# Kernel tuning notes

Hardware: AMD Instinct MI355X
Metric: run time of the kernel (lower is better)

Reference implementation:

```python
import jax, jax.numpy as jnp
import numpy as np

B, S, D = 4, 4096, 2048
K, H = 64, 32
HD = K // H  # 2
LN_EPS = 1e-5


def setup_inputs() -> dict:
    key = jax.random.key(0)
    ks = jax.random.split(key, 8)
    def xavier(k, shape):
        fan_in, fan_out = shape[1], shape[0]
        lim = float(np.sqrt(6.0 / (fan_in + fan_out)))
        return jax.random.uniform(k, shape, jnp.float32, -lim, lim)
    return {
        "x": jax.random.normal(ks[0], (B, S, D), jnp.float32),
        "norm_w": jnp.ones((D,), jnp.float32),
        "norm_b": jnp.zeros((D,), jnp.float32),
        "qkv_w": xavier(ks[1], (3 * K, D)),
        "qkv_b": jnp.zeros((3 * K,), jnp.float32),
        "fm_w": xavier(ks[2], (HD, HD)),
        "fm_b": jnp.zeros((HD,), jnp.float32),
        "out_w": xavier(ks[3], (D, K)),
        "out_b": jnp.zeros((D,), jnp.float32),
    }


def reference(x, norm_w, norm_b, qkv_w, qkv_b, fm_w, fm_b, out_w, out_b):
    # LayerNorm
    mu = jnp.mean(x, axis=-1, keepdims=True)
    var = jnp.var(x, axis=-1, keepdims=True)
    xn = (x - mu) * jax.lax.rsqrt(var + LN_EPS) * norm_w + norm_b
    # QKV projection: [B,S,3K]
    qkv = xn @ qkv_w.T + qkv_b
    q, k, v = jnp.split(qkv, 3, axis=-1)
    # [B,S,K] -> [B,H,S,hd]
    def heads(t):
        return t.reshape(B, S, H, HD).transpose(0, 2, 1, 3)
    q, k, v = heads(q), heads(k), heads(v)
    # feature map: ReLU(Linear)
    q = jax.nn.relu(q @ fm_w.T + fm_b)
    k = jax.nn.relu(k @ fm_w.T + fm_b)
    # linear attention: kv state [B,H,hd,hd]
    kv = jnp.einsum('bhsd,bhse->bhde', k, v)
    attn = jnp.einsum('bhsd,bhde->bhse', q, kv)
    k_sum = jnp.sum(k, axis=2)                      # [B,H,hd]
    q_k_sum = jnp.einsum('bhsd,bhd->bhs', q, k_sum)[..., None]
    attn = attn / (q_k_sum + 1e-8)
    # merge heads -> [B,S,K]
    attn = attn.transpose(0, 2, 1, 3).reshape(B, S, K)
    out = attn @ out_w.T + out_b
    return x + out
```

## Files before the change

### kernel.cpp

```cpp
#include <hip/hip_runtime.h>
#include <hip/hip_bf16.h>
#include <stdint.h>

typedef unsigned short ushort_t;

#define BB 4
#define SS 4096
#define DD 2048
#define KKC 64
#define HH 32
#define NT (BB*SS)
#define NQKV 192
#define QB 32

typedef float f32x4 __attribute__((ext_vector_type(4)));
typedef short s16x8 __attribute__((ext_vector_type(8)));

__device__ __forceinline__ ushort_t f2bf(float f) {
    union { float f; uint32_t u; } c; c.f = f;
    uint32_t u = c.u + 0x7fffu + ((c.u >> 16) & 1u);
    return (ushort_t)(u >> 16);
}
__device__ __forceinline__ float bf2f(ushort_t b) {
    union { uint32_t u; float f; } c; c.u = (uint32_t)b << 16; return c.f;
}

__device__ __forceinline__ uint32_t cvtpk(float lo, float hi) {
    uint32_t r;
    asm("v_cvt_pk_bf16_f32 %0, %1, %2" : "=v"(r) : "v"(lo), "v"(hi));
    return r;
}

__device__ __forceinline__ void mfma16(f32x4& d, s16x8 a, s16x8 b) {
    asm volatile("v_mfma_f32_16x16x32_bf16 %0, %1, %2, %0" : "+v"(d) : "v"(a), "v"(b));
}

__device__ __forceinline__ void gload_lds16(const void* gsrc, void* ldst) {
    __builtin_amdgcn_global_load_lds(
        (const __attribute__((address_space(1))) unsigned int*)gsrc,
        (__attribute__((address_space(3))) unsigned int*)ldst,
        16, 0, 0);
}

__global__ __launch_bounds__(256) void k_pre(
    const float* __restrict__ qkv_w, const float* __restrict__ nw,
    const float* __restrict__ out_w,
    ushort_t* __restrict__ W1, ushort_t* __restrict__ W2) {
    int E = blockIdx.x * 256 + threadIdx.x;
    if (E < 49152) {
        int lane = E & 63; int rest = E >> 6;
        int f = rest % 12, g = rest / 12;
        int col = f * 16 + (lane & 15);
        int k0 = g * 32 + 8 * (lane >> 4);
        const float* src = qkv_w + (size_t)col * DD + k0;
        const float* wp = nw + k0;
        union { ushort_t u[8]; uint4 v; } cv;
        #pragma unroll
        for (int e = 0; e < 8; ++e) cv.u[e] = f2bf(src[e] * wp[e]);
        *(uint4*)(W1 + (size_t)E * 8) = cv.v;
    } else {
        int E2 = E - 49152;
        int lane = E2 & 63; int rest = E2 >> 6;
        int kk = rest & 1, F = rest >> 1;
        int n = F * 16 + (lane & 15);
        int k0 = kk * 32 + 8 * (lane >> 4);
        const float* src = out_w + (size_t)n * KKC + k0;
        union { ushort_t u[8]; uint4 v; } cv;
        #pragma unroll
        for (int e = 0; e < 8; ++e) cv.u[e] = f2bf(src[e]);
        *(uint4*)(W2 + (size_t)E2 * 8) = cv.v;
    }
}

__global__ __launch_bounds__(256) void k_colsum(
    const float* __restrict__ qkv_w, const float* __restrict__ nw,
    const float* __restrict__ nb, const float* __restrict__ qkv_b,
    float* __restrict__ S, float* __restrict__ qb2) {
    int col = blockIdx.x * 4 + (threadIdx.x >> 6);
    int lane = threadIdx.x & 63;
    float s = 0.f, qb = 0.f;
    for (int j = 0; j < 32; ++j) {
        int k = j * 64 + lane;
        float w = qkv_w[(size_t)col * DD + k];
        s += bf2f(f2bf(w * nw[k]));
        qb += nb[k] * w;
    }
    #pragma unroll
    for (int off = 32; off >= 1; off >>= 1) {
        s += __shfl_xor(s, off);
        qb += __shfl_xor(qb, off);
    }
    if (lane == 0) { S[col] = s; qb2[col] = qb + qkv_b[col]; }
}

__global__ __launch_bounds__(512, 4) void k_qkv(
    const float* __restrict__ x, const ushort_t* __restrict__ W1,
    const float* __restrict__ S, const float* __restrict__ qb2,
    const float* __restrict__ fm_w, const float* __restrict__ fm_b,
    float* __restrict__ qfeat,
    float* __restrict__ kvpart)
{
    __shared__ __align__(16) union {
        struct {
            ushort_t b[2][1536 * 8];
            float xs[2][QB * 64];
        } st;
        float cep[QB][NQKV];
    } sm;
    __shared__ float kvred[32][16][6];
    __shared__ float stats4[4][32][2];
    __shared__ float stats[QB][2];

    const int tid = threadIdx.x;
    const int wave = tid >> 6, lane = tid & 63;
    const int rg = wave & 1, ch = wave >> 1;
    const int m0 = blockIdx.x * QB;

    const int rloc = rg * 16 + (lane & 15);
    const int q4 = lane >> 4;
    const int swz = rloc & 7;

    f32x4 acc[3];
    #pragma unroll
    for (int j = 0; j < 3; ++j) acc[j] = (f32x4){0.f, 0.f, 0.f, 0.f};
    float st1 = 0.f, st2 = 0.f;

    const int lidx = wave * 64 + lane;
    const int xrow = lidx >> 4;
    const int xslot = (lidx & 15) ^ (xrow & 7);
    const size_t xgbase = (size_t)(m0 + xrow) * DD + xslot * 4;

    #pragma unroll
    for (int i = 0; i < 3; ++i) {
        int ebase = i * 512 + wave * 64;
        gload_lds16((const char*)W1 + ((size_t)0 * 1536 + ebase + lane) * 16,
                    (char*)sm.st.b[0] + (size_t)ebase * 16);
    }
    gload_lds16(x + xgbase + 0 * 64, (char*)sm.st.xs[0] + (size_t)wave * 1024);

    for (int t = 0; t < 32; ++t) {
        const int cur = t & 1;
        __syncthreads();
        if (t < 31) {
            #pragma unroll
            for (int i = 0; i < 3; ++i) {
                int ebase = i * 512 + wave * 64;
                gload_lds16((const char*)W1 + ((size_t)(t + 1) * 1536 + ebase + lane) * 16,
                            (char*)sm.st.b[cur ^ 1] + (size_t)ebase * 16);
            }
            gload_lds16(x + xgbase + (size_t)(t + 1) * 64,
                        (char*)sm.st.xs[cur ^ 1] + (size_t)wave * 1024);
        }
        s16x8 afr[2];
        const bool doStats = ((t & 3) == ch);
        #pragma unroll
        for (int kb = 0; kb < 2; ++kb) {
            int sg = kb * 8 + 2 * q4;
            const float* base = sm.st.xs[cur] + rloc * 64;
            float4 v0 = *(const float4*)(base + (sg ^ swz) * 4);
            float4 v1 = *(const float4*)(base + ((sg + 1) ^ swz) * 4);
            if (doStats) {
                st1 += v0.x + v0.y + v0.z + v0.w + v1.x + v1.y + v1.z + v1.w;
                st2 += v0.x*v0.x + v0.y*v0.y + v0.z*v0.z + v0.w*v0.w
                     + v1.x*v1.x + v1.y*v1.y + v1.z*v1.z + v1.w*v1.w;
            }
            union { uint32_t w[4]; s16x8 v; } cv;
            cv.w[0] = cvtpk(v0.x, v0.y);
            cv.w[1] = cvtpk(v0.z, v0.w);
            cv.w[2] = cvtpk(v1.x, v1.y);
            cv.w[3] = cvtpk(v1.z, v1.w);
            afr[kb] = cv.v;
        }
        #pragma unroll
        for (int j = 0; j < 3; ++j) {
            s16x8 b0 = ((const s16x8*)sm.st.b[cur])[(0 * 12 + ch * 3 + j) * 64 + lane];
            s16x8 b1 = ((const s16x8*)sm.st.b[cur])[(1 * 12 + ch * 3 + j) * 64 + lane];
            mfma16(acc[j], afr[0], b0);
            mfma16(acc[j], afr[1], b1);
        }
    }

    st1 += __shfl_xor(st1, 16); st2 += __shfl_xor(st2, 16);
    st1 += __shfl_xor(st1, 32); st2 += __shfl_xor(st2, 32);
    if (lane < 16) { stats4[ch][rg * 16 + lane][0] = st1; stats4[ch][rg * 16 + lane][1] = st2; }
    __syncthreads();

    #pragma unroll
    for (int j = 0; j < 3; ++j) {
        int col = (ch * 3 + j) * 16 + (lane & 15);
        int rbase = rg * 16 + (lane >> 4) * 4;
        #pragma unroll
        for (int r = 0; r < 4; ++r)
            sm.cep[rbase + r][col] = acc[j][r];
    }
    if (tid < 32) {
        float s1 = stats4[0][tid][0] + stats4[1][tid][0] + stats4[2][tid][0] + stats4[3][tid][0];
        float s2 = stats4[0][tid][1] + stats4[1][tid][1] + stats4[2][tid][1] + stats4[3][tid][1];
        float mu = s1 * (1.f / DD);
        float var = s2 * (1.f / DD) - mu * mu;
        stats[tid][0] = mu;
        stats[tid][1] = rsqrtf(var + 1e-5f);
    }
    __syncthreads();

    const int h = tid & 31, gg = tid >> 5;
    const float fm00 = fm_w[0], fm01 = fm_w[1], fm10 = fm_w[2], fm11 = fm_w[3];
    const float fb0 = fm_b[0], fb1 = fm_b[1];
    const float Sq0 = S[2*h],      Sq1 = S[2*h+1],      cq0 = qb2[2*h],      cq1 = qb2[2*h+1];
    const float Sk0 = S[64+2*h],   Sk1 = S[64+2*h+1],   ck0 = qb2[64+2*h],   ck1 = qb2[64+2*h+1];
    const float Sv0 = S[128+2*h],  Sv1 = S[128+2*h+1],  cv0 = qb2[128+2*h],  cv1 = qb2[128+2*h+1];
    float kv00=0, kv01=0, kv10=0, kv11=0, ks0=0, ks1=0;
    #pragma unroll
    for (int i = 0; i < 2; ++i) {
        int tt = gg * 2 + i;
        float mu = stats[tt][0], rs = stats[tt][1];
        float f = mu * rs;
        float q0 = rs * sm.cep[tt][2*h]      - f * Sq0 + cq0;
        float q1 = rs * sm.cep[tt][2*h+1]    - f * Sq1 + cq1;
        float k0 = rs * sm.cep[tt][64+2*h]   - f * Sk0 + ck0;
        float k1 = rs * sm.cep[tt][64+2*h+1] - f * Sk1 + ck1;
        float v0 = rs * sm.cep[tt][128+2*h]  - f * Sv0 + cv0;
        float v1 = rs * sm.cep[tt][128+2*h+1]- f * Sv1 + cv1;
        float qp0 = fmaxf(fm00*q0 + fm01*q1 + fb0, 0.f);
        float qp1 = fmaxf(fm10*q0 + fm11*q1 + fb1, 0.f);
        float kp0 = fmaxf(fm00*k0 + fm01*k1 + fb0, 0.f);
        float kp1 = fmaxf(fm10*k0 + fm11*k1 + fb1, 0.f);
        *(float2*)(qfeat + (size_t)(m0 + tt) * KKC + 2*h) = make_float2(qp0, qp1);
        kv00 += kp0*v0; kv01 += kp0*v1; kv10 += kp1*v0; kv11 += kp1*v1;
        ks0 += kp0; ks1 += kp1;
    }
    kvred[h][gg][0]=kv00; kvred[h][gg][1]=kv01; kvred[h][gg][2]=kv10;
    kvred[h][gg][3]=kv11; kvred[h][gg][4]=ks0;  kvred[h][gg][5]=ks1;
    __syncthreads();
    if (tid < 192) {
        int h2 = tid / 6, j = tid % 6;
        float s = 0.f;
        #pragma unroll
        for (int g2 = 0; g2 < 16; ++g2) s += kvred[h2][g2][j];
        kvpart[(size_t)blockIdx.x * 192 + tid] = s;
    }
}

__global__ void k_red(const float* __restrict__ kvpart, float* __restrict__ kvstate) {
    int idx = blockIdx.x * 256 + threadIdx.x;
    if (idx >= BB * HH * 6) return;
    int b = idx / 192, r = idx % 192;
    float s = 0.f;
    for (int blk = 0; blk < 128; ++blk)
        s += kvpart[(size_t)(b * 128 + blk) * 192 + r];
    kvstate[idx] = s;
}

#define CEP_STRIDE 260
__global__ __launch_bounds__(512, 4) void k_out(
    const float* __restrict__ qfeat, const float* __restrict__ kvstate,
    const ushort_t* __restrict__ W2, const float* __restrict__ out_b,
    const float* __restrict__ x, float* __restrict__ out) {
    __shared__ float skv[192];
    __shared__ __align__(16) float cep[32 * CEP_STRIDE];
    const int tid = threadIdx.x, wave = tid >> 6, lane = tid & 63;
    const int rg = wave & 1, cq = wave >> 1;
    const int mb = blockIdx.x >> 1, nb = blockIdx.x & 1;
    const int m0 = mb * 32;
    const int n0 = nb * 1024;
    const int b = m0 >> 12;
    if (tid < 192) skv[tid] = kvstate[b * 192 + tid];

    const int arow = m0 + rg * 16 + (lane & 15);
    const int ksub = 8 * (lane >> 4);
    float4 qa0 = *(const float4*)(qfeat + (size_t)arow * KKC + ksub);
    float4 qa1 = *(const float4*)(qfeat + (size_t)arow * KKC + ksub + 4);
    float4 qb0 = *(const float4*)(qfeat + (size_t)arow * KKC + 32 + ksub);
    float4 qb1 = *(const float4*)(qfeat + (size_t)arow * KKC + 32 + ksub + 4);
    __syncthreads();

    union { ushort_t u[8]; s16x8 v; } ca, cb;
    {
        float qs[8] = {qa0.x,qa0.y,qa0.z,qa0.w,qa1.x,qa1.y,qa1.z,qa1.w};
        float rs[8] = {qb0.x,qb0.y,qb0.z,qb0.w,qb1.x,qb1.y,qb1.z,qb1.w};
        #pragma unroll
        for (int e = 0; e < 8; e += 2) {
            int h = (ksub + e) >> 1;
            const float* kv = skv + h * 6;
            float q0 = qs[e], q1 = qs[e+1];
            float inv = 1.f / (q0 * kv[4] + q1 * kv[5] + 1e-8f);
            ca.u[e]   = f2bf((q0 * kv[0] + q1 * kv[2]) * inv);
            ca.u[e+1] = f2bf((q0 * kv[1] + q1 * kv[3]) * inv);
            const float* kw = skv + (h + 16) * 6;
            float p0 = rs[e], p1 = rs[e+1];
            float iw = 1.f / (p0 * kw[4] + p1 * kw[5] + 1e-8f);
            cb.u[e]   = f2bf((p0 * kw[0] + p1 * kw[2]) * iw);
            cb.u[e+1] = f2bf((p0 * kw[1] + p1 * kw[3]) * iw);
        }
    }

    f32x4 acc[16];
    #pragma unroll
    for (int j = 0; j < 16; ++j) acc[j] = (f32x4){0.f, 0.f, 0.f, 0.f};
    #pragma unroll
    for (int j = 0; j < 16; ++j) {
        int Fg = (n0 >> 4) + cq + 4 * j;
        s16x8 b0 = *(const s16x8*)(W2 + ((size_t)(Fg * 2 + 0) * 64 + lane) * 8);
        s16x8 b1 = *(const s16x8*)(W2 + ((size_t)(Fg * 2 + 1) * 64 + lane) * 8);
        mfma16(acc[j], ca.v, b0);
        mfma16(acc[j], cb.v, b1);
    }

    const int wrow = rg * 16 + 4 * (lane >> 4);
    #pragma unroll
    for (int n = 0; n < 4; ++n) {
        #pragma unroll
        for (int i = 0; i < 4; ++i) {
            int col = cq * 16 + i * 64 + (lane & 15);
            #pragma unroll
            for (int r = 0; r < 4; ++r)
                cep[(wrow + r) * CEP_STRIDE + col] = acc[4 * n + i][r];
        }
        __syncthreads();
        #pragma unroll
        for (int p = 0; p < 4; ++p) {
            int row = p * 8 + (tid >> 6);
            int c4 = tid & 63;
            float4 c = *(const float4*)(cep + row * CEP_STRIDE + c4 * 4);
            int gcol = n0 + n * 256 + c4 * 4;
            size_t off = (size_t)(m0 + row) * DD + gcol;
            float4 xr = *(const float4*)(x + off);
            float4 ob = *(const float4*)(out_b + gcol);
            float4 o;
            o.x = c.x + ob.x + xr.x; o.y = c.y + ob.y + xr.y;
            o.z = c.z + ob.z + xr.z; o.w = c.w + ob.w + xr.w;
            *(float4*)(out + off) = o;
        }
        __syncthreads();
    }
}

extern "C" void kernel_launch(void* const* d_in, const int* in_sizes, int n_in,
                              void* d_out, int out_size, void* d_ws, size_t ws_size,
                              hipStream_t stream) {
    const float* x     = (const float*)d_in[0];
    const float* nw    = (const float*)d_in[1];
    const float* nb    = (const float*)d_in[2];
    const float* qkv_w = (const float*)d_in[3];
    const float* qkv_b = (const float*)d_in[4];
    const float* fm_w  = (const float*)d_in[5];
    const float* fm_b  = (const float*)d_in[6];
    const float* out_w = (const float*)d_in[7];
    const float* out_b = (const float*)d_in[8];
    float* out = (float*)d_out;

    char* ws = (char*)d_ws;
    ushort_t* W1 = (ushort_t*)ws;     ws += (size_t)NQKV * DD * 2;
    ushort_t* W2 = (ushort_t*)ws;     ws += (size_t)DD * KKC * 2;
    float* qfeat = (float*)ws;        ws += (size_t)NT * KKC * 4;
    float* kvpart = (float*)ws;       ws += (size_t)512 * 192 * 4;
    float* kvstate = (float*)ws;      ws += (size_t)BB * HH * 6 * 4;
    float* Svec = (float*)ws;         ws += (size_t)NQKV * 4;
    float* qb2 = (float*)ws;          ws += (size_t)NQKV * 4;

    k_pre<<<256, 256, 0, stream>>>(qkv_w, nw, out_w, W1, W2);
    k_colsum<<<48, 256, 0, stream>>>(qkv_w, nw, nb, qkv_b, Svec, qb2);
    k_qkv<<<NT / QB, 512, 0, stream>>>(x, W1, Svec, qb2, fm_w, fm_b, qfeat, kvpart);
    k_red<<<3, 256, 0, stream>>>(kvpart, kvstate);
    k_out<<<(NT / 32) * 2, 512, 0, stream>>>(qfeat, kvstate, W2, out_b, x, out);
}
```

Measured before the change: 126.2 us.

## Double QKV row tile and stream weight fragments straight into registers

The QKV projection kernel now handles 64 rows per block instead of 32. Each wave computes 6 column fragments, so more rows share every weight fragment. Weight tiles are no longer staged through LDS. They are loaded from global memory directly into register double buffers, while x stays double-buffered in LDS with an unrolled ping-pong loop. The LayerNorm statistics work is split across two wave groups, and the partial KV reduction is adjusted to the halved block count. The cost is higher register pressure (launch bounds lowered to 2 blocks per SM) and half as many blocks, which may leave the GPU underfilled.

```diff
diff --git a/kernel.cpp b/kernel.cpp
--- a/kernel.cpp
+++ b/kernel.cpp
@@ -11,7 +11,7 @@
 #define HH 32
 #define NT (BB*SS)
 #define NQKV 192
-#define QB 32
+#define QB 64
 
 typedef float f32x4 __attribute__((ext_vector_type(4)));
 typedef short s16x8 __attribute__((ext_vector_type(8)));
@@ -93,7 +93,7 @@
     if (lane == 0) { S[col] = s; qb2[col] = qb + qkv_b[col]; }
 }
 
-__global__ __launch_bounds__(512, 4) void k_qkv(
+__global__ __launch_bounds__(512, 2) void k_qkv(
     const float* __restrict__ x, const ushort_t* __restrict__ W1,
     const float* __restrict__ S, const float* __restrict__ qb2,
     const float* __restrict__ fm_w, const float* __restrict__ fm_b,
@@ -101,101 +101,126 @@
     float* __restrict__ kvpart)
 {
     __shared__ __align__(16) union {
-        struct {
-            ushort_t b[2][1536 * 8];
-            float xs[2][QB * 64];
-        } st;
+        float xs[2][QB * 16 * 4];
         float cep[QB][NQKV];
     } sm;
     __shared__ float kvred[32][16][6];
-    __shared__ float stats4[4][32][2];
+    __shared__ float stats2[2][QB][2];
     __shared__ float stats[QB][2];
 
     const int tid = threadIdx.x;
     const int wave = tid >> 6, lane = tid & 63;
-    const int rg = wave & 1, ch = wave >> 1;
+    const int rg = wave & 3, ch = wave >> 2;
     const int m0 = blockIdx.x * QB;
 
     const int rloc = rg * 16 + (lane & 15);
     const int q4 = lane >> 4;
     const int swz = rloc & 7;
 
-    f32x4 acc[3];
-    #pragma unroll
-    for (int j = 0; j < 3; ++j) acc[j] = (f32x4){0.f, 0.f, 0.f, 0.f};
+    const int idx0 = wave * 64 + lane;
+    const int idx1 = 512 + idx0;
+    const int row0 = idx0 >> 4, row1 = idx1 >> 4;
+    const size_t xg0 = (size_t)(m0 + row0) * DD + (((idx0 & 15) ^ (row0 & 7)) * 4);
+    const size_t xg1 = (size_t)(m0 + row1) * DD + (((idx1 & 15) ^ (row1 & 7)) * 4);
+    const int xd0 = (wave * 64) * 16;
+    const int xd1 = (512 + wave * 64) * 16;
+
+    const s16x8* __restrict__ Wp = (const s16x8*)W1;
+    const int fbase = ch * 6;
+
+    f32x4 acc[6];
+    #pragma unroll
+    for (int j = 0; j < 6; ++j) acc[j] = (f32x4){0.f, 0.f, 0.f, 0.f};
     float st1 = 0.f, st2 = 0.f;
 
-    const int lidx = wave * 64 + lane;
-    const int xrow = lidx >> 4;
-    const int xslot = (lidx & 15) ^ (xrow & 7);
-    const size_t xgbase = (size_t)(m0 + xrow) * DD + xslot * 4;
-
-    #pragma unroll
-    for (int i = 0; i < 3; ++i) {
-        int ebase = i * 512 + wave * 64;
-        gload_lds16((const char*)W1 + ((size_t)0 * 1536 + ebase + lane) * 16,
-                    (char*)sm.st.b[0] + (size_t)ebase * 16);
-    }
-    gload_lds16(x + xgbase + 0 * 64, (char*)sm.st.xs[0] + (size_t)wave * 1024);
-
-    for (int t = 0; t < 32; ++t) {
-        const int cur = t & 1;
+#define STAGE_X(T, BUF) do { \
+        gload_lds16(x + xg0 + (size_t)(T) * 64, (char*)sm.xs[BUF] + xd0); \
+        gload_lds16(x + xg1 + (size_t)(T) * 64, (char*)sm.xs[BUF] + xd1); \
+    } while (0)
+
+#define LOAD_B(T, DST) do { \
+        _Pragma("unroll") \
+        for (int kb = 0; kb < 2; ++kb) { \
+            _Pragma("unroll") \
+            for (int j = 0; j < 6; ++j) \
+                DST[kb][j] = Wp[(((size_t)((T) * 2 + kb) * 12) + fbase + j) * 64 + lane]; \
+        } \
+    } while (0)
+
+#define AFRAG(BUF, DOSTATS) \
+        s16x8 afr0, afr1; \
+        { \
+            const float* base = sm.xs[BUF] + rloc * 64; \
+            int sg0 = 2 * q4, sg1 = 8 + 2 * q4; \
+            float4 a0 = *(const float4*)(base + ((sg0    ) ^ swz) * 4); \
+            float4 a1 = *(const float4*)(base + ((sg0 + 1) ^ swz) * 4); \
+            float4 b0 = *(const float4*)(base + ((sg1    ) ^ swz) * 4); \
+            float4 b1 = *(const float4*)(base + ((sg1 + 1) ^ swz) * 4); \
+            if (DOSTATS) { \
+                st1 += a0.x+a0.y+a0.z+a0.w + a1.x+a1.y+a1.z+a1.w \
+                     + b0.x+b0.y+b0.z+b0.w + b1.x+b1.y+b1.z+b1.w; \
+                st2 += a0.x*a0.x+a0.y*a0.y+a0.z*a0.z+a0.w*a0.w \
+                     + a1.x*a1.x+a1.y*a1.y+a1.z*a1.z+a1.w*a1.w \
+                     + b0.x*b0.x+b0.y*b0.y+b0.z*b0.z+b0.w*b0.w \
+                     + b1.x*b1.x+b1.y*b1.y+b1.z*b1.z+b1.w*b1.w; \
+            } \
+            union { uint32_t w[4]; s16x8 v; } c0, c1; \
+            c0.w[0] = cvtpk(a0.x, a0.y); c0.w[1] = cvtpk(a0.z, a0.w); \
+            c0.w[2] = cvtpk(a1.x, a1.y); c0.w[3] = cvtpk(a1.z, a1.w); \
+            c1.w[0] = cvtpk(b0.x, b0.y); c1.w[1] = cvtpk(b0.z, b0.w); \
+            c1.w[2] = cvtpk(b1.x, b1.y); c1.w[3] = cvtpk(b1.z, b1.w); \
+            afr0 = c0.v; afr1 = c1.v; \
+        }
+
+    s16x8 bA[2][6], bB[2][6];
+
+    STAGE_X(0, 0);
+    LOAD_B(0, bA);
+
+    for (int tp = 0; tp < 16; ++tp) {
+        const int t0 = 2 * tp, t1 = 2 * tp + 1;
         __syncthreads();
-        if (t < 31) {
+        STAGE_X(t0 + 1, 1);
+        LOAD_B(t0 + 1, bB);
+        {
+            AFRAG(0, (ch == 0));
             #pragma unroll
-            for (int i = 0; i < 3; ++i) {
-                int ebase = i * 512 + wave * 64;
-                gload_lds16((const char*)W1 + ((size_t)(t + 1) * 1536 + ebase + lane) * 16,
-                            (char*)sm.st.b[cur ^ 1] + (size_t)ebase * 16);
+            for (int j = 0; j < 6; ++j) {
+                mfma16(acc[j], afr0, bA[0][j]);
+                mfma16(acc[j], afr1, bA[1][j]);
             }
-            gload_lds16(x + xgbase + (size_t)(t + 1) * 64,
-                        (char*)sm.st.xs[cur ^ 1] + (size_t)wave * 1024);
-        }
-        s16x8 afr[2];
-        const bool doStats = ((t & 3) == ch);
-        #pragma unroll
-        for (int kb = 0; kb < 2; ++kb) {
-            int sg = kb * 8 + 2 * q4;
-            const float* base = sm.st.xs[cur] + rloc * 64;
-            float4 v0 = *(const float4*)(base + (sg ^ swz) * 4);
-            float4 v1 = *(const float4*)(base + ((sg + 1) ^ swz) * 4);
-            if (doStats) {
-                st1 += v0.x + v0.y + v0.z + v0.w + v1.x + v1.y + v1.z + v1.w;
-                st2 += v0.x*v0.x + v0.y*v0.y + v0.z*v0.z + v0.w*v0.w
-                     + v1.x*v1.x + v1.y*v1.y + v1.z*v1.z + v1.w*v1.w;
+        }
+        __syncthreads();
+        if (t1 < 31) {
+            STAGE_X(t1 + 1, 0);
+            LOAD_B(t1 + 1, bA);
+        }
+        {
+            AFRAG(1, (ch == 1));
+            #pragma unroll
+            for (int j = 0; j < 6; ++j) {
+                mfma16(acc[j], afr0, bB[0][j]);
+                mfma16(acc[j], afr1, bB[1][j]);
             }
-            union { uint32_t w[4]; s16x8 v; } cv;
-            cv.w[0] = cvtpk(v0.x, v0.y);
-            cv.w[1] = cvtpk(v0.z, v0.w);
-            cv.w[2] = cvtpk(v1.x, v1.y);
-            cv.w[3] = cvtpk(v1.z, v1.w);
-            afr[kb] = cv.v;
-        }
-        #pragma unroll
-        for (int j = 0; j < 3; ++j) {
-            s16x8 b0 = ((const s16x8*)sm.st.b[cur])[(0 * 12 + ch * 3 + j) * 64 + lane];
-            s16x8 b1 = ((const s16x8*)sm.st.b[cur])[(1 * 12 + ch * 3 + j) * 64 + lane];
-            mfma16(acc[j], afr[0], b0);
-            mfma16(acc[j], afr[1], b1);
         }
     }
 
     st1 += __shfl_xor(st1, 16); st2 += __shfl_xor(st2, 16);
     st1 += __shfl_xor(st1, 32); st2 += __shfl_xor(st2, 32);
-    if (lane < 16) { stats4[ch][rg * 16 + lane][0] = st1; stats4[ch][rg * 16 + lane][1] = st2; }
+    if (lane < 16) { stats2[ch][rloc][0] = st1; stats2[ch][rloc][1] = st2; }
     __syncthreads();
 
     #pragma unroll
-    for (int j = 0; j < 3; ++j) {
-        int col = (ch * 3 + j) * 16 + (lane & 15);
+    for (int j = 0; j < 6; ++j) {
+        int col = (fbase + j) * 16 + (lane & 15);
         int rbase = rg * 16 + (lane >> 4) * 4;
         #pragma unroll
         for (int r = 0; r < 4; ++r)
             sm.cep[rbase + r][col] = acc[j][r];
     }
-    if (tid < 32) {
-        float s1 = stats4[0][tid][0] + stats4[1][tid][0] + stats4[2][tid][0] + stats4[3][tid][0];
-        float s2 = stats4[0][tid][1] + stats4[1][tid][1] + stats4[2][tid][1] + stats4[3][tid][1];
+    if (tid < QB) {
+        float s1 = stats2[0][tid][0] + stats2[1][tid][0];
+        float s2 = stats2[0][tid][1] + stats2[1][tid][1];
         float mu = s1 * (1.f / DD);
         float var = s2 * (1.f / DD) - mu * mu;
         stats[tid][0] = mu;
@@ -211,8 +236,8 @@
     const float Sv0 = S[128+2*h],  Sv1 = S[128+2*h+1],  cv0 = qb2[128+2*h],  cv1 = qb2[128+2*h+1];
     float kv00=0, kv01=0, kv10=0, kv11=0, ks0=0, ks1=0;
     #pragma unroll
-    for (int i = 0; i < 2; ++i) {
-        int tt = gg * 2 + i;
+    for (int i = 0; i < 4; ++i) {
+        int tt = gg * 4 + i;
         float mu = stats[tt][0], rs = stats[tt][1];
         float f = mu * rs;
         float q0 = rs * sm.cep[tt][2*h]      - f * Sq0 + cq0;
@@ -239,6 +264,9 @@
         for (int g2 = 0; g2 < 16; ++g2) s += kvred[h2][g2][j];
         kvpart[(size_t)blockIdx.x * 192 + tid] = s;
     }
+#undef STAGE_X
+#undef LOAD_B
+#undef AFRAG
 }
 
 __global__ void k_red(const float* __restrict__ kvpart, float* __restrict__ kvstate) {
@@ -246,8 +274,8 @@
     if (idx >= BB * HH * 6) return;
     int b = idx / 192, r = idx % 192;
     float s = 0.f;
-    for (int blk = 0; blk < 128; ++blk)
-        s += kvpart[(size_t)(b * 128 + blk) * 192 + r];
+    for (int blk = 0; blk < 64; ++blk)
+        s += kvpart[(size_t)(b * 64 + blk) * 192 + r];
     kvstate[idx] = s;
 }
 
@@ -353,7 +381,7 @@
     ushort_t* W1 = (ushort_t*)ws;     ws += (size_t)NQKV * DD * 2;
     ushort_t* W2 = (ushort_t*)ws;     ws += (size_t)DD * KKC * 2;
     float* qfeat = (float*)ws;        ws += (size_t)NT * KKC * 4;
-    float* kvpart = (float*)ws;       ws += (size_t)512 * 192 * 4;
+    float* kvpart = (float*)ws;       ws += (size_t)256 * 192 * 4;
     float* kvstate = (float*)ws;      ws += (size_t)BB * HH * 6 * 4;
     float* Svec = (float*)ws;         ws += (size_t)NQKV * 4;
     float* qb2 = (float*)ws;          ws += (size_t)NQKV * 4;
```

New measurement: 127.8 us. Within noise of the previous version (+1.2%).

## Split x cast/stats into separate kernel and load MFMA operands directly from global

Applied to the files above, without the earlier changes.

Adds a k_cast kernel that reads x once, computes LayerNorm stats, and writes a bf16 copy laid out in MFMA fragment order. k_qkv then reads bf16 A and W1 fragments straight from global memory into registers with software double-buffering, instead of staging through LDS with global_load_lds. It uses 256 threads, each wave covering 6 column tiles. This removes LDS staging and barriers from the GEMM loop, but adds a full extra write and read of a bf16 copy of x (about 64MB) through memory.

```diff
diff --git a/kernel.cpp b/kernel.cpp
--- a/kernel.cpp
+++ b/kernel.cpp
@@ -11,7 +11,6 @@
 #define HH 32
 #define NT (BB*SS)
 #define NQKV 192
-#define QB 32
 
 typedef float f32x4 __attribute__((ext_vector_type(4)));
 typedef short s16x8 __attribute__((ext_vector_type(8)));
@@ -33,13 +32,6 @@
 
 __device__ __forceinline__ void mfma16(f32x4& d, s16x8 a, s16x8 b) {
     asm volatile("v_mfma_f32_16x16x32_bf16 %0, %1, %2, %0" : "+v"(d) : "v"(a), "v"(b));
-}
-
-__device__ __forceinline__ void gload_lds16(const void* gsrc, void* ldst) {
-    __builtin_amdgcn_global_load_lds(
-        (const __attribute__((address_space(1))) unsigned int*)gsrc,
-        (__attribute__((address_space(3))) unsigned int*)ldst,
-        16, 0, 0);
 }
 
 __global__ __launch_bounds__(256) void k_pre(
@@ -93,113 +85,111 @@
     if (lane == 0) { S[col] = s; qb2[col] = qb + qkv_b[col]; }
 }
 
-__global__ __launch_bounds__(512, 4) void k_qkv(
-    const float* __restrict__ x, const ushort_t* __restrict__ W1,
+__global__ __launch_bounds__(256) void k_cast(
+    const float* __restrict__ x, ushort_t* __restrict__ XB,
+    float* __restrict__ stats_g) {
+    __shared__ float sp[2][16][16];
+    const int tid = threadIdx.x;
+    const int m0 = blockIdx.x * 16;
+    const int row = tid & 15;
+    const int q = (tid >> 4) & 3;
+    const size_t R64 = (size_t)blockIdx.x * 64;
+    const float* xrow = x + (size_t)(m0 + row) * DD;
+    float st1 = 0.f, st2 = 0.f;
+    #pragma unroll
+    for (int it = 0; it < 16; ++it) {
+        int g = it * 4 + (tid >> 6);
+        int k0 = g * 32 + 8 * q;
+        const float4* xp = (const float4*)(xrow + k0);
+        float4 v0 = xp[0], v1 = xp[1];
+        st1 += v0.x + v0.y + v0.z + v0.w + v1.x + v1.y + v1.z + v1.w;
+        st2 += v0.x*v0.x + v0.y*v0.y + v0.z*v0.z + v0.w*v0.w
+             + v1.x*v1.x + v1.y*v1.y + v1.z*v1.z + v1.w*v1.w;
+        union { uint32_t w[4]; uint4 u; } cv;
+        cv.w[0] = cvtpk(v0.x, v0.y); cv.w[1] = cvtpk(v0.z, v0.w);
+        cv.w[2] = cvtpk(v1.x, v1.y); cv.w[3] = cvtpk(v1.z, v1.w);
+        *(uint4*)(XB + ((R64 + g) * 64 + (tid & 63)) * 8) = cv.u;
+    }
+    sp[0][row][tid >> 4] = st1;
+    sp[1][row][tid >> 4] = st2;
+    __syncthreads();
+    if (tid < 16) {
+        float s1 = 0.f, s2 = 0.f;
+        #pragma unroll
+        for (int i = 0; i < 16; ++i) { s1 += sp[0][tid][i]; s2 += sp[1][tid][i]; }
+        float mu = s1 * (1.f / DD);
+        float var = s2 * (1.f / DD) - mu * mu;
+        stats_g[(size_t)(m0 + tid) * 2]     = mu;
+        stats_g[(size_t)(m0 + tid) * 2 + 1] = rsqrtf(var + 1e-5f);
+    }
+}
+
+__global__ __launch_bounds__(256) void k_qkv(
+    const ushort_t* __restrict__ XB, const ushort_t* __restrict__ W1,
+    const float* __restrict__ stats_g,
     const float* __restrict__ S, const float* __restrict__ qb2,
     const float* __restrict__ fm_w, const float* __restrict__ fm_b,
     float* __restrict__ qfeat,
     float* __restrict__ kvpart)
 {
-    __shared__ __align__(16) union {
-        struct {
-            ushort_t b[2][1536 * 8];
-            float xs[2][QB * 64];
-        } st;
-        float cep[QB][NQKV];
-    } sm;
-    __shared__ float kvred[32][16][6];
-    __shared__ float stats4[4][32][2];
-    __shared__ float stats[QB][2];
+    __shared__ float cep[32][NQKV];
+    __shared__ float kvred[32][8][6];
 
     const int tid = threadIdx.x;
     const int wave = tid >> 6, lane = tid & 63;
-    const int rg = wave & 1, ch = wave >> 1;
-    const int m0 = blockIdx.x * QB;
-
-    const int rloc = rg * 16 + (lane & 15);
-    const int q4 = lane >> 4;
-    const int swz = rloc & 7;
-
-    f32x4 acc[3];
-    #pragma unroll
-    for (int j = 0; j < 3; ++j) acc[j] = (f32x4){0.f, 0.f, 0.f, 0.f};
-    float st1 = 0.f, st2 = 0.f;
-
-    const int lidx = wave * 64 + lane;
-    const int xrow = lidx >> 4;
-    const int xslot = (lidx & 15) ^ (xrow & 7);
-    const size_t xgbase = (size_t)(m0 + xrow) * DD + xslot * 4;
-
-    #pragma unroll
-    for (int i = 0; i < 3; ++i) {
-        int ebase = i * 512 + wave * 64;
-        gload_lds16((const char*)W1 + ((size_t)0 * 1536 + ebase + lane) * 16,
-                    (char*)sm.st.b[0] + (size_t)ebase * 16);
-    }
-    gload_lds16(x + xgbase + 0 * 64, (char*)sm.st.xs[0] + (size_t)wave * 1024);
-
-    for (int t = 0; t < 32; ++t) {
-        const int cur = t & 1;
-        __syncthreads();
-        if (t < 31) {
-            #pragma unroll
-            for (int i = 0; i < 3; ++i) {
-                int ebase = i * 512 + wave * 64;
-                gload_lds16((const char*)W1 + ((size_t)(t + 1) * 1536 + ebase + lane) * 16,
-                            (char*)sm.st.b[cur ^ 1] + (size_t)ebase * 16);
-            }
-            gload_lds16(x + xgbase + (size_t)(t + 1) * 64,
-                        (char*)sm.st.xs[cur ^ 1] + (size_t)wave * 1024);
-        }
-        s16x8 afr[2];
-        const bool doStats = ((t & 3) == ch);
-        #pragma unroll
-        for (int kb = 0; kb < 2; ++kb) {
-            int sg = kb * 8 + 2 * q4;
-            const float* base = sm.st.xs[cur] + rloc * 64;
-            float4 v0 = *(const float4*)(base + (sg ^ swz) * 4);
-            float4 v1 = *(const float4*)(base + ((sg + 1) ^ swz) * 4);
-            if (doStats) {
-                st1 += v0.x + v0.y + v0.z + v0.w + v1.x + v1.y + v1.z + v1.w;
-                st2 += v0.x*v0.x + v0.y*v0.y + v0.z*v0.z + v0.w*v0.w
-                     + v1.x*v1.x + v1.y*v1.y + v1.z*v1.z + v1.w*v1.w;
-            }
-            union { uint32_t w[4]; s16x8 v; } cv;
-            cv.w[0] = cvtpk(v0.x, v0.y);
-            cv.w[1] = cvtpk(v0.z, v0.w);
-            cv.w[2] = cvtpk(v1.x, v1.y);
-            cv.w[3] = cvtpk(v1.z, v1.w);
-            afr[kb] = cv.v;
-        }
-        #pragma unroll
-        for (int j = 0; j < 3; ++j) {
-            s16x8 b0 = ((const s16x8*)sm.st.b[cur])[(0 * 12 + ch * 3 + j) * 64 + lane];
-            s16x8 b1 = ((const s16x8*)sm.st.b[cur])[(1 * 12 + ch * 3 + j) * 64 + lane];
-            mfma16(acc[j], afr[0], b0);
-            mfma16(acc[j], afr[1], b1);
-        }
-    }
-
-    st1 += __shfl_xor(st1, 16); st2 += __shfl_xor(st2, 16);
-    st1 += __shfl_xor(st1, 32); st2 += __shfl_xor(st2, 32);
-    if (lane < 16) { stats4[ch][rg * 16 + lane][0] = st1; stats4[ch][rg * 16 + lane][1] = st2; }
-    __syncthreads();
-
-    #pragma unroll
-    for (int j = 0; j < 3; ++j) {
-        int col = (ch * 3 + j) * 16 + (lane & 15);
+    const int rg = wave & 1, chh = wave >> 1;
+    const int m0 = blockIdx.x * 32;
+    const int R = blockIdx.x * 2 + rg;
+    const int fbase = chh * 6;
+
+    const s16x8* __restrict__ Ap = (const s16x8*)XB + (size_t)R * 64 * 64 + lane;
+    const s16x8* __restrict__ Wp = (const s16x8*)W1;
+
+    f32x4 acc[6];
+    #pragma unroll
+    for (int j = 0; j < 6; ++j) acc[j] = (f32x4){0.f, 0.f, 0.f, 0.f};
+
+#define LOAD_A(T, DST) do { \
+        DST[0] = Ap[(size_t)(2 * (T)    ) * 64]; \
+        DST[1] = Ap[(size_t)(2 * (T) + 1) * 64]; \
+    } while (0)
+#define LOAD_B(T, DST) do { \
+        _Pragma("unroll") \
+        for (int kb = 0; kb < 2; ++kb) { \
+            _Pragma("unroll") \
+            for (int j = 0; j < 6; ++j) \
+                DST[kb][j] = Wp[(((size_t)(2 * (T) + kb) * 12) + fbase + j) * 64 + lane]; \
+        } \
+    } while (0)
+
+    s16x8 aA[2], aB[2], bA[2][6], bB[2][6];
+    LOAD_A(0, aA); LOAD_B(0, bA);
+
+    for (int tp = 0; tp < 16; ++tp) {
+        const int t1 = 2 * tp + 1;
+        LOAD_A(t1, aB); LOAD_B(t1, bB);
+        #pragma unroll
+        for (int j = 0; j < 6; ++j) {
+            mfma16(acc[j], aA[0], bA[0][j]);
+            mfma16(acc[j], aA[1], bA[1][j]);
+        }
+        if (t1 < 31) { LOAD_A(t1 + 1, aA); LOAD_B(t1 + 1, bA); }
+        #pragma unroll
+        for (int j = 0; j < 6; ++j) {
+            mfma16(acc[j], aB[0], bB[0][j]);
+            mfma16(acc[j], aB[1], bB[1][j]);
+        }
+    }
+#undef LOAD_A
+#undef LOAD_B
+
+    #pragma unroll
+    for (int j = 0; j < 6; ++j) {
+        int col = (fbase + j) * 16 + (lane & 15);
         int rbase = rg * 16 + (lane >> 4) * 4;
         #pragma unroll
         for (int r = 0; r < 4; ++r)
-            sm.cep[rbase + r][col] = acc[j][r];
-    }
-    if (tid < 32) {
-        float s1 = stats4[0][tid][0] + stats4[1][tid][0] + stats4[2][tid][0] + stats4[3][tid][0];
-        float s2 = stats4[0][tid][1] + stats4[1][tid][1] + stats4[2][tid][1] + stats4[3][tid][1];
-        float mu = s1 * (1.f / DD);
-        float var = s2 * (1.f / DD) - mu * mu;
-        stats[tid][0] = mu;
-        stats[tid][1] = rsqrtf(var + 1e-5f);
+            cep[rbase + r][col] = acc[j][r];
     }
     __syncthreads();
 
@@ -211,16 +201,17 @@
     const float Sv0 = S[128+2*h],  Sv1 = S[128+2*h+1],  cv0 = qb2[128+2*h],  cv1 = qb2[128+2*h+1];
     float kv00=0, kv01=0, kv10=0, kv11=0, ks0=0, ks1=0;
     #pragma unroll
-    for (int i = 0; i < 2; ++i) {
-        int tt = gg * 2 + i;
-        float mu = stats[tt][0], rs = stats[tt][1];
+    for (int i = 0; i < 4; ++i) {
+        int tt = gg * 4 + i;
+        float mu = stats_g[(size_t)(m0 + tt) * 2];
+        float rs = stats_g[(size_t)(m0 + tt) * 2 + 1];
         float f = mu * rs;
-        float q0 = rs * sm.cep[tt][2*h]      - f * Sq0 + cq0;
-        float q1 = rs * sm.cep[tt][2*h+1]    - f * Sq1 + cq1;
-        float k0 = rs * sm.cep[tt][64+2*h]   - f * Sk0 + ck0;
-        float k1 = rs * sm.cep[tt][64+2*h+1] - f * Sk1 + ck1;
-        float v0 = rs * sm.cep[tt][128+2*h]  - f * Sv0 + cv0;
-        float v1 = rs * sm.cep[tt][128+2*h+1]- f * Sv1 + cv1;
+        float q0 = rs * cep[tt][2*h]      - f * Sq0 + cq0;
+        float q1 = rs * cep[tt][2*h+1]    - f * Sq1 + cq1;
+        float k0 = rs * cep[tt][64+2*h]   - f * Sk0 + ck0;
+        float k1 = rs * cep[tt][64+2*h+1] - f * Sk1 + ck1;
+        float v0 = rs * cep[tt][128+2*h]  - f * Sv0 + cv0;
+        float v1 = rs * cep[tt][128+2*h+1]- f * Sv1 + cv1;
         float qp0 = fmaxf(fm00*q0 + fm01*q1 + fb0, 0.f);
         float qp1 = fmaxf(fm10*q0 + fm11*q1 + fb1, 0.f);
         float kp0 = fmaxf(fm00*k0 + fm01*k1 + fb0, 0.f);
@@ -236,7 +227,7 @@
         int h2 = tid / 6, j = tid % 6;
         float s = 0.f;
         #pragma unroll
-        for (int g2 = 0; g2 < 16; ++g2) s += kvred[h2][g2][j];
+        for (int g2 = 0; g2 < 8; ++g2) s += kvred[h2][g2][j];
         kvpart[(size_t)blockIdx.x * 192 + tid] = s;
     }
 }
@@ -352,6 +343,8 @@
     char* ws = (char*)d_ws;
     ushort_t* W1 = (ushort_t*)ws;     ws += (size_t)NQKV * DD * 2;
     ushort_t* W2 = (ushort_t*)ws;     ws += (size_t)DD * KKC * 2;
+    ushort_t* XB = (ushort_t*)ws;     ws += (size_t)NT * DD * 2;
+    float* stats = (float*)ws;        ws += (size_t)NT * 2 * 4;
     float* qfeat = (float*)ws;        ws += (size_t)NT * KKC * 4;
     float* kvpart = (float*)ws;       ws += (size_t)512 * 192 * 4;
     float* kvstate = (float*)ws;      ws += (size_t)BB * HH * 6 * 4;
@@ -360,7 +353,8 @@
 
     k_pre<<<256, 256, 0, stream>>>(qkv_w, nw, out_w, W1, W2);
     k_colsum<<<48, 256, 0, stream>>>(qkv_w, nw, nb, qkv_b, Svec, qb2);
-    k_qkv<<<NT / QB, 512, 0, stream>>>(x, W1, Svec, qb2, fm_w, fm_b, qfeat, kvpart);
+    k_cast<<<NT / 16, 256, 0, stream>>>(x, XB, stats);
+    k_qkv<<<NT / 32, 256, 0, stream>>>(XB, W1, stats, Svec, qb2, fm_w, fm_b, qfeat, kvpart);
     k_red<<<3, 256, 0, stream>>>(kvpart, kvstate);
     k_out<<<(NT / 32) * 2, 512, 0, stream>>>(qfeat, kvstate, W2, out_b, x, out);
 }
```

New measurement: 155.8 us. +23.4%, slower.
